# Kernel optimization log

Hardware: AMD Instinct MI355X
Metric: run time of the kernel (lower is better)

Reference implementation:

```python
import jax, jax.numpy as jnp
import numpy as np

D_MODEL = 1024
NUM_HEADS = 16
D_K = D_MODEL // NUM_HEADS
HEADS_DIST = [4, 4, 2, 2, 4]  # [token, statement, data_flow, control_flow, standard]
HYP_DF = 5.0
HYP_CF = 5.0
NEG_INF = -1000000000.0
B, S = 4, 1024


def _head_group_weights():
    # one-hot-per-group weight vectors of length NUM_HEADS
    ws = []
    start = 0
    for n in HEADS_DIST:
        w = np.zeros(NUM_HEADS, dtype=np.float32)
        w[start:start + n] = 1.0
        ws.append(jnp.asarray(w))
        start += n
    return ws  # tok_w, stmt_w, df_w, cf_w, std_w


def setup_inputs() -> dict:
    key = jax.random.key(0)
    ks = jax.random.split(key, 12)
    f32 = jnp.float32
    inp = {
        'Q': jax.random.normal(ks[0], (B, S, D_MODEL), f32),
        'K': jax.random.normal(ks[1], (B, S, D_MODEL), f32),
        'V': jax.random.normal(ks[2], (B, S, D_MODEL), f32),
        'token': jax.random.randint(ks[3], (B, S, S), 0, 2).astype(f32),
        'statement': jax.random.randint(ks[4], (B, S, S), 0, 2).astype(f32),
        'data_flow': jax.random.randint(ks[5], (B, S, S), 0, 2).astype(f32),
        'control_flow': jax.random.randint(ks[6], (B, S, S), 0, 2).astype(f32),
        'zero_matrix': jnp.zeros((B, S, S), f32),
        'mask': jax.random.randint(ks[7], (B, 1, S, S), 0, 2).astype(jnp.int32),
        # linear layer params (torch nn.Linear: y = x @ W.T + b)
        'Wq': jax.random.normal(ks[8], (D_MODEL, D_MODEL), f32) * 0.02,
        'bq': jnp.zeros((D_MODEL,), f32),
        'Wk': jax.random.normal(ks[9], (D_MODEL, D_MODEL), f32) * 0.02,
        'bk': jnp.zeros((D_MODEL,), f32),
        'Wv': jax.random.normal(ks[10], (D_MODEL, D_MODEL), f32) * 0.02,
        'bv': jnp.zeros((D_MODEL,), f32),
        'Wo': jax.random.normal(ks[11], (D_MODEL, D_MODEL), f32) * 0.02,
        'bo': jnp.zeros((D_MODEL,), f32),
    }
    return inp


def _split_heads(x):
    b, s, _ = x.shape
    return x.reshape(b, s, NUM_HEADS, D_K).transpose(0, 2, 1, 3)  # (B,H,S,dk)


def reference(Q, K, V, token, statement, data_flow, control_flow, zero_matrix,
              mask, Wq, bq, Wk, bk, Wv, bv, Wo, bo):
    tok_w, stmt_w, df_w, cf_w, _ = _head_group_weights()

    Qh = _split_heads(Q @ Wq.T + bq)
    Kh = _split_heads(K @ Wk.T + bk)
    Vh = _split_heads(V @ Wv.T + bv)

    scores = jnp.einsum('bhqd,bhkd->bhqk', Qh, Kh) / jnp.sqrt(jnp.float32(D_K))

    # local mask: -1e9 * token for token-heads, -1e9 * statement for statement-heads,
    # zero_matrix (zeros) elsewhere — expressed via per-head group weights instead of
    # the original redundant stack.
    w = lambda v: v[None, :, None, None]  # (1,H,1,1)
    local_mask = NEG_INF * (w(tok_w) * token[:, None] + w(stmt_w) * statement[:, None])
    # global enhance: |scores * (hyp_df*data_flow | hyp_cf*control_flow)| on their heads
    enhance_adj = (HYP_DF * w(df_w) * data_flow[:, None]
                   + HYP_CF * w(cf_w) * control_flow[:, None])
    global_enhance = jnp.abs(enhance_adj * scores)

    scores = scores + local_mask + global_enhance
    scores = jnp.where(mask == 0, NEG_INF, scores)

    probs = jax.nn.softmax(scores, axis=-1)  # (B,H,S,S)
    ctx = jnp.einsum('bhqk,bhkd->bhqd', probs, Vh)
    out = ctx.transpose(0, 2, 1, 3).reshape(B, S, D_MODEL)
    return out @ Wo.T + bo
```

## Files before the change

### kernel.cpp

```cpp
#include <hip/hip_runtime.h>
#include <stdint.h>

typedef unsigned short u16;
typedef unsigned int   u32;
typedef unsigned char  u8;
typedef __attribute__((ext_vector_type(4))) float f32x4;
typedef __attribute__((ext_vector_type(8))) __bf16 bf16x8;
typedef __attribute__((ext_vector_type(2))) unsigned int u32x2;
typedef __attribute__((ext_vector_type(4))) unsigned int u32x4;

#define MFMA16(a, b, c) __builtin_amdgcn_mfma_f32_16x16x32_bf16((a), (b), (c), 0, 0, 0)

__device__ __forceinline__ u16 f2bf(float f) {
  u32 u = __float_as_uint(f);
  return (u16)((u + 0x7fffu + ((u >> 16) & 1u)) >> 16);
}

__device__ __forceinline__ void gl_lds16(const void* g, void* l) {
  __builtin_amdgcn_global_load_lds((const __attribute__((address_space(1))) u32*)g,
                                   (__attribute__((address_space(3))) u32*)l, 16, 0, 0);
}

__device__ __forceinline__ u32 cvtpk(float a, float b) {
  u32 r;
  asm("v_cvt_pk_bf16_f32 %0, %1, %2" : "=v"(r) : "v"(a), "v"(b));
  return r;
}

__device__ __forceinline__ float exp2_hw(float x) {
  float r;
  asm("v_exp_f32 %0, %1" : "=v"(r) : "v"(x));
  return r;
}

__device__ __forceinline__ void plswap32(u32& x, u32& y) {
  u32x2 r = __builtin_amdgcn_permlane32_swap(x, y, false, false);
  x = r.x; y = r.y;
}
__device__ __forceinline__ void plswap16(u32& x, u32& y) {
  u32x2 r = __builtin_amdgcn_permlane16_swap(x, y, false, false);
  x = r.x; y = r.y;
}

__device__ __forceinline__ float redmax_lg(float v) {
  u32 x = __float_as_uint(v), y = x;
  plswap16(x, y);
  float m = fmaxf(__uint_as_float(x), __uint_as_float(y));
  u32 a = __float_as_uint(m), b = a;
  plswap32(a, b);
  return fmaxf(__uint_as_float(a), __uint_as_float(b));
}
__device__ __forceinline__ float redsum_lg(float v) {
  u32 x = __float_as_uint(v), y = x;
  plswap16(x, y);
  float m = __uint_as_float(x) + __uint_as_float(y);
  u32 a = __float_as_uint(m), b = a;
  plswap32(a, b);
  return __uint_as_float(a) + __uint_as_float(b);
}

__device__ __forceinline__ u32 pbit(float t, float s, float d, float c, int m) {
  const u32 nm = (m == 0) ? 1u : 0u;
  u32 r = (t != 0.0f ? 1u : 0u) | (s != 0.0f ? 2u : 0u) | (d != 0.0f ? 4u : 0u) |
          (c != 0.0f ? 8u : 0u) | ((1u - nm) << 4);
  r |= (((t != 0.0f ? 1u : 0u) | nm) << 5) | (((s != 0.0f ? 1u : 0u) | nm) << 6) | (nm << 7);
  return r;
}

__global__ void __launch_bounds__(256) prep_kernel(
    const float4* __restrict__ Q, const float4* __restrict__ K, const float4* __restrict__ V,
    const float4* __restrict__ Wq, const float4* __restrict__ Wk, const float4* __restrict__ Wv,
    const float4* __restrict__ Wo, ushort4* __restrict__ oQ, ushort4* __restrict__ oK,
    ushort4* __restrict__ oV, ushort4* __restrict__ oWq, ushort4* __restrict__ oWk,
    ushort4* __restrict__ oWv, ushort4* __restrict__ oWo,
    const float4* __restrict__ tok, const float4* __restrict__ st, const float4* __restrict__ df,
    const float4* __restrict__ cf, const int4* __restrict__ msk, u32* __restrict__ pko) {
  const int bid = blockIdx.x;
  float4 v;
  if (bid < 2048) {
    const int i = bid * 512 + threadIdx.x;
#pragma unroll
    for (int u = 0; u < 2; u++) {
      const int k = i + u * 256;
      v = Q[k]; oQ[k] = make_ushort4(f2bf(v.x), f2bf(v.y), f2bf(v.z), f2bf(v.w));
      v = K[k]; oK[k] = make_ushort4(f2bf(v.x), f2bf(v.y), f2bf(v.z), f2bf(v.w));
      v = V[k]; oV[k] = make_ushort4(f2bf(v.x), f2bf(v.y), f2bf(v.z), f2bf(v.w));
    }
  } else if (bid < 2560) {
    const int j = (bid - 2048) * 512 + threadIdx.x;
#pragma unroll
    for (int u = 0; u < 2; u++) {
      const int k = j + u * 256;
      v = Wq[k]; oWq[k] = make_ushort4(f2bf(v.x), f2bf(v.y), f2bf(v.z), f2bf(v.w));
      v = Wk[k]; oWk[k] = make_ushort4(f2bf(v.x), f2bf(v.y), f2bf(v.z), f2bf(v.w));
      v = Wv[k]; oWv[k] = make_ushort4(f2bf(v.x), f2bf(v.y), f2bf(v.z), f2bf(v.w));
      v = Wo[k]; oWo[k] = make_ushort4(f2bf(v.x), f2bf(v.y), f2bf(v.z), f2bf(v.w));
    }
  } else {
    const int i = (bid - 2560) * 256 + threadIdx.x;
    const int b = i >> 18, rem = i & 262143, q = rem >> 8, k4 = rem & 255;
    const int t = k4 >> 4, nk = (k4 >> 2) & 3, lg = k4 & 3;
    const u32 widx = ((u32)(b * 64 + (q >> 4)) * 16 + t) * 256 + (q & 15) * 16 + lg * 4 + nk;
    float4 vt = tok[i], vs = st[i], vd = df[i], vc = cf[i];
    int4 vm = msk[i];
    u32 b0 = pbit(vt.x, vs.x, vd.x, vc.x, vm.x);
    u32 b1 = pbit(vt.y, vs.y, vd.y, vc.y, vm.y);
    u32 b2 = pbit(vt.z, vs.z, vd.z, vc.z, vm.z);
    u32 b3 = pbit(vt.w, vs.w, vd.w, vc.w, vm.w);
    pko[widx] = b0 | (b1 << 8) | (b2 << 16) | (b3 << 24);
  }
}

__global__ void __launch_bounds__(256) gemm_qkv(const u16* __restrict__ Abase, const u16* __restrict__ Wbase,
                                                const float* __restrict__ bq, const float* __restrict__ bk,
                                                const float* __restrict__ bv, u16* __restrict__ Obase) {
  __shared__ u16 smA[128 * 32];
  __shared__ u16 smB[128 * 32];
  const int fb = blockIdx.x;
  const int lid = (fb & 7) * 96 + (fb >> 3);
  const int z = lid >> 8;
  const int m0 = ((lid & 255) >> 3) * 128;
  const int n0 = (lid & 7) * 128;
  const u16* A = Abase + (size_t)z * 4194304;
  const u16* W = Wbase + (size_t)z * 1048576;
  const float* bias = (z == 0) ? bq : (z == 1) ? bk : bv;
  u16* Out = Obase + (size_t)z * 4194304;
  const int t = threadIdx.x;
  const int w = t >> 6, l = t & 63;
  const int l15 = l & 15, lg = l >> 4;
  const int wr = w >> 1, wc = w & 1;
  f32x4 acc[4][4] = {};
  const int srow = w * 16 + (l >> 2);
  const int scol = (l & 3) * 8;
  const u16* Ab = A + (size_t)(m0 + srow) * 1024 + scol;
  const u16* Wb = W + (size_t)(n0 + srow) * 1024 + scol;
  u16* sA0 = smA + srow * 32 + scol;
  u16* sB0 = smB + srow * 32 + scol;
  for (int kk = 0; kk < 1024; kk += 32) {
    gl_lds16(Ab + kk, sA0);
    gl_lds16(Ab + kk + (size_t)64 * 1024, sA0 + 64 * 32);
    gl_lds16(Wb + kk, sB0);
    gl_lds16(Wb + kk + (size_t)64 * 1024, sB0 + 64 * 32);
    __syncthreads();
    bf16x8 af[4], bv_[4];
#pragma unroll
    for (int i = 0; i < 4; i++) af[i] = *(const bf16x8*)(smA + (wr * 64 + i * 16 + l15) * 32 + lg * 8);
#pragma unroll
    for (int i = 0; i < 4; i++) bv_[i] = *(const bf16x8*)(smB + (wc * 64 + i * 16 + l15) * 32 + lg * 8);
#pragma unroll
    for (int i = 0; i < 4; i++)
#pragma unroll
      for (int j = 0; j < 4; j++) acc[i][j] = MFMA16(af[i], bv_[j], acc[i][j]);
    __syncthreads();
  }
#pragma unroll
  for (int j = 0; j < 4; j++) {
    const int n = n0 + wc * 64 + j * 16 + l15;
    const float bvj = bias[n];
#pragma unroll
    for (int i = 0; i < 4; i++) {
      const int mbase = m0 + wr * 64 + i * 16 + lg * 4;
      if (z < 2) {
#pragma unroll
        for (int r = 0; r < 4; r++) {
          const int m = mbase + r;
          Out[((size_t)((m >> 10) * 16 + (n >> 6)) << 16) + (size_t)(m & 1023) * 64 + (n & 63)] =
              f2bf(acc[i][j][r] + bvj);
        }
      } else {
        size_t off = ((size_t)((mbase >> 10) * 16 + (n >> 6)) << 16) + (size_t)(n & 63) * 1024 + (mbase & 1023);
        *(ushort4*)(Out + off) = make_ushort4(f2bf(acc[i][j][0] + bvj), f2bf(acc[i][j][1] + bvj),
                                              f2bf(acc[i][j][2] + bvj), f2bf(acc[i][j][3] + bvj));
      }
    }
  }
}

__global__ void __launch_bounds__(256) gemm_out(const u16* __restrict__ A, const u16* __restrict__ W,
                                                const float* __restrict__ bias, float* __restrict__ Out) {
  __shared__ u16 smA[128 * 32];
  __shared__ u16 smB[128 * 32];
  const int fb = blockIdx.x;
  const int lid = (fb & 7) * 32 + (fb >> 3);
  const int m0 = (lid >> 3) * 128;
  const int n0 = (lid & 7) * 128;
  const int t = threadIdx.x;
  const int w = t >> 6, l = t & 63;
  const int l15 = l & 15, lg = l >> 4;
  const int wr = w >> 1, wc = w & 1;
  f32x4 acc[4][4] = {};
  const int srow = w * 16 + (l >> 2);
  const int scol = (l & 3) * 8;
  const u16* Ab = A + (size_t)(m0 + srow) * 1024 + scol;
  const u16* Wb = W + (size_t)(n0 + srow) * 1024 + scol;
  u16* sA0 = smA + srow * 32 + scol;
  u16* sB0 = smB + srow * 32 + scol;
  for (int kk = 0; kk < 1024; kk += 32) {
    gl_lds16(Ab + kk, sA0);
    gl_lds16(Ab + kk + (size_t)64 * 1024, sA0 + 64 * 32);
    gl_lds16(Wb + kk, sB0);
    gl_lds16(Wb + kk + (size_t)64 * 1024, sB0 + 64 * 32);
    __syncthreads();
    bf16x8 af[4], bv_[4];
#pragma unroll
    for (int i = 0; i < 4; i++) af[i] = *(const bf16x8*)(smA + (wr * 64 + i * 16 + l15) * 32 + lg * 8);
#pragma unroll
    for (int i = 0; i < 4; i++) bv_[i] = *(const bf16x8*)(smB + (wc * 64 + i * 16 + l15) * 32 + lg * 8);
#pragma unroll
    for (int i = 0; i < 4; i++)
#pragma unroll
      for (int j = 0; j < 4; j++) acc[i][j] = MFMA16(af[i], bv_[j], acc[i][j]);
    __syncthreads();
  }
#pragma unroll
  for (int j = 0; j < 4; j++) {
    const int n = n0 + wc * 64 + j * 16 + l15;
    const float bvj = bias[n];
#pragma unroll
    for (int i = 0; i < 4; i++) {
      const int mbase = m0 + wr * 64 + i * 16 + lg * 4;
#pragma unroll
      for (int r = 0; r < 4; r++) Out[(size_t)(mbase + r) * 1024 + n] = acc[i][j][r] + bvj;
    }
  }
}

__global__ void __launch_bounds__(256) attn_kernel(const u16* __restrict__ Qp, const u16* __restrict__ Kp,
                                                   const u16* __restrict__ Vt, const u8* __restrict__ pack,
                                                   u16* __restrict__ ctx) {
  __shared__ u16 smK[2][4096];
  __shared__ u16 smV[2][4096];
  const float SCL  = 0.18033688011112042f;
  const float NEGL = -1.44269504e9f;
  const int tid = threadIdx.x;
  const int w = tid >> 6, l = tid & 63;
  const int l15 = l & 15, lg = l >> 4;
  const int f = blockIdx.x;
  const int swz = (f & 7) * 128 + (f >> 3);
  const int bh = swz >> 4, bx = swz & 15;
  const int b = bh >> 4, h = bh & 15;
  const int q0 = bx * 64 + w * 16;
  const bool enh = (h >= 8 && h < 12);
  const u32 kbit = (h < 4) ? 0x20u : (h < 8) ? 0x40u : 0x80u;
  const u32 ebit = (h < 10) ? 0x04u : 0x08u;
  const u32 kb_[4] = {kbit, kbit << 8, kbit << 16, kbit << 24};
  const u32 eb_[4] = {ebit, ebit << 8, ebit << 16, ebit << 24};
  const size_t hb = (size_t)bh << 16;

  bf16x8 qf[2];
#pragma unroll
  for (int ks = 0; ks < 2; ks++)
    qf[ks] = *(const bf16x8*)(Qp + hb + (size_t)(q0 + l15) * 64 + ks * 32 + lg * 8);

  const int srow = w * 16 + (l >> 3);
  const int schunk = (l & 7) ^ (l >> 3);
  const u16* Ksrc = Kp + hb + (size_t)srow * 64 + schunk * 8;
  const u16* Vsrc = Vt + hb + (size_t)srow * 1024 + schunk * 8;
  const int c0 = (lg ^ (l15 & 7)) * 8;
  const u8* pkq = pack + ((size_t)((b * 64 + bx * 4 + w) * 16)) * 1024 + (l15 * 4 + lg) * 16;

  gl_lds16(Ksrc, &smK[0][w * 1024]);
  gl_lds16(Ksrc + 512, &smK[0][w * 1024 + 512]);
  gl_lds16(Vsrc, &smV[0][w * 1024]);
  gl_lds16(Vsrc + 8192, &smV[0][w * 1024 + 512]);
  uint4 pk_next = *(const uint4*)(pkq);

  f32x4 octx[4] = {};
  float mrun = -3.0e38f, lrun = 0.0f;

  for (int t = 0; t < 16; t++) {
    __syncthreads();
    const uint4 pkc = pk_next;
    if (t < 15) {
      const int kb = (t + 1) * 64;
      const int nb = (t + 1) & 1;
      gl_lds16(Ksrc + (size_t)kb * 64, &smK[nb][w * 1024]);
      gl_lds16(Ksrc + (size_t)kb * 64 + 512, &smK[nb][w * 1024 + 512]);
      gl_lds16(Vsrc + kb, &smV[nb][w * 1024]);
      gl_lds16(Vsrc + kb + 8192, &smV[nb][w * 1024 + 512]);
      pk_next = *(const uint4*)(pkq + (t + 1) * 1024);
    }
    const u16* bK = smK[t & 1];
    const u16* bV = smV[t & 1];
    f32x4 sc[4];
#pragma unroll
    for (int nk = 0; nk < 4; nk++) {
      const u16* kr = bK + (nk * 16 + l15) * 64;
      bf16x8 kf0 = *(const bf16x8*)(kr + c0);
      bf16x8 kf1 = *(const bf16x8*)(kr + (c0 ^ 32));
      f32x4 z = {0.0f, 0.0f, 0.0f, 0.0f};
      z = MFMA16(kf0, qf[0], z);
      z = MFMA16(kf1, qf[1], z);
      sc[nk] = z;
    }
    const u32 pkw[4] = {pkc.x, pkc.y, pkc.z, pkc.w};
#pragma unroll
    for (int nk = 0; nk < 4; nk++)
#pragma unroll
      for (int r = 0; r < 4; r++) {
        float s = sc[nk][r] * SCL;
        if (enh) s = (pkw[nk] & eb_[r]) ? __builtin_fmaf(fabsf(s), 5.0f, s) : s;
        sc[nk][r] = (pkw[nk] & kb_[r]) ? NEGL : s;
      }
    float mx[4];
#pragma unroll
    for (int nk = 0; nk < 4; nk++)
      mx[nk] = fmaxf(fmaxf(sc[nk][0], sc[nk][1]), fmaxf(sc[nk][2], sc[nk][3]));
    float smax = fmaxf(fmaxf(mx[0], mx[1]), fmaxf(mx[2], mx[3]));
    smax = redmax_lg(smax);
    const bool defer = __all(smax - mrun <= 11.0f);
    const float mn = defer ? mrun : fmaxf(mrun, smax);
    float psum = 0.0f;
#pragma unroll
    for (int nk = 0; nk < 4; nk++)
#pragma unroll
      for (int r = 0; r < 4; r++) {
        float p = exp2_hw(sc[nk][r] - mn);
        sc[nk][r] = p;
        psum += p;
      }
    psum = redsum_lg(psum);
    if (defer) {
      lrun += psum;
    } else {
      const float so = exp2_hw(mrun - mn);
      lrun = lrun * so + psum;
      mrun = mn;
#pragma unroll
      for (int nd = 0; nd < 4; nd++)
#pragma unroll
        for (int r = 0; r < 4; r++) octx[nd][r] *= so;
    }
#pragma unroll
    for (int kk = 0; kk < 2; kk++) {
      u32 a0 = cvtpk(sc[2 * kk][0], sc[2 * kk][1]);
      u32 a1 = cvtpk(sc[2 * kk][2], sc[2 * kk][3]);
      u32 b0 = cvtpk(sc[2 * kk + 1][0], sc[2 * kk + 1][1]);
      u32 b1 = cvtpk(sc[2 * kk + 1][2], sc[2 * kk + 1][3]);
      plswap32(a0, b0);
      plswap32(a1, b1);
      plswap16(a0, b0);
      plswap16(a1, b1);
      u32x4 wv = {a0, a1, b0, b1};
      bf16x8 pfrag = __builtin_bit_cast(bf16x8, wv);
#pragma unroll
      for (int nd = 0; nd < 4; nd++) {
        bf16x8 vf = *(const bf16x8*)(bV + (nd * 16 + l15) * 64 + (c0 ^ (kk * 32)));
        octx[nd] = MFMA16(vf, pfrag, octx[nd]);
      }
    }
  }
  const float inv = 1.0f / lrun;
  u16* cb = ctx + (size_t)b * 1048576 + (size_t)(q0 + l15) * 1024 + h * 64 + lg * 4;
#pragma unroll
  for (int nd = 0; nd < 4; nd++) {
    *(ushort4*)(cb + nd * 16) = make_ushort4(f2bf(octx[nd][0] * inv), f2bf(octx[nd][1] * inv),
                                             f2bf(octx[nd][2] * inv), f2bf(octx[nd][3] * inv));
  }
}

extern "C" void kernel_launch(void* const* d_in, const int* in_sizes, int n_in,
                              void* d_out, int out_size, void* d_ws, size_t ws_size,
                              hipStream_t stream) {
  (void)in_sizes; (void)n_in; (void)out_size; (void)ws_size;
  const float* Q  = (const float*)d_in[0];
  const float* K  = (const float*)d_in[1];
  const float* V  = (const float*)d_in[2];
  const float* tok = (const float*)d_in[3];
  const float* st  = (const float*)d_in[4];
  const float* df  = (const float*)d_in[5];
  const float* cf  = (const float*)d_in[6];
  const int*   msk = (const int*)d_in[8];
  const float* Wq = (const float*)d_in[9];
  const float* bq = (const float*)d_in[10];
  const float* Wk = (const float*)d_in[11];
  const float* bk = (const float*)d_in[12];
  const float* Wv = (const float*)d_in[13];
  const float* bv = (const float*)d_in[14];
  const float* Wo = (const float*)d_in[15];
  const float* bo = (const float*)d_in[16];

  char* ws = (char*)d_ws;
  const size_t MB = 1ull << 20;
  u16* Qbf = (u16*)(ws);
  u16* Wqb = (u16*)(ws + 24 * MB);
  u8*  pkQ = (u8*)(ws + 32 * MB);
  u16* Qh  = (u16*)(ws + 36 * MB);
  u16* ctx = (u16*)(ws + 60 * MB);
  u16* Kbf = Qbf + 4194304;
  u16* Vbf = Qbf + 8388608;
  u16* Wkb = Wqb + 1048576;
  u16* Wvb = Wqb + 2097152;
  u16* Wob = Wqb + 3145728;

  prep_kernel<<<6656, 256, 0, stream>>>(
      (const float4*)Q, (const float4*)K, (const float4*)V, (const float4*)Wq, (const float4*)Wk,
      (const float4*)Wv, (const float4*)Wo, (ushort4*)Qbf, (ushort4*)Kbf, (ushort4*)Vbf,
      (ushort4*)Wqb, (ushort4*)Wkb, (ushort4*)Wvb, (ushort4*)Wob,
      (const float4*)tok, (const float4*)st, (const float4*)df, (const float4*)cf,
      (const int4*)msk, (u32*)pkQ);
  gemm_qkv<<<768, 256, 0, stream>>>(Qbf, Wqb, bq, bk, bv, Qh);
  attn_kernel<<<1024, 256, 0, stream>>>(Qh, Qh + 4194304, Qh + 8388608, pkQ, ctx);
  gemm_out<<<256, 256, 0, stream>>>(ctx, Wob, bo, (float*)d_out);
}
```

Before: 148.8 us.

## Fuse fp32-to-bf16 conversion into GEMM loads with register prefetch

Removes the separate prep pass that converted Q/K/V and all weights to bf16. The QKV and output GEMMs now read fp32 directly into registers, convert to bf16, and store to LDS. The next tile is prefetched into registers during the MFMA work, and the loop barrier is restructured. This saves a full extra read and write of the activations and weights, but the GEMMs now read twice as many bytes from global memory and replace direct global-to-LDS loads with register staging.

```diff
diff --git a/kernel.cpp b/kernel.cpp
--- a/kernel.cpp
+++ b/kernel.cpp
@@ -67,51 +67,25 @@
   return r;
 }
 
-__global__ void __launch_bounds__(256) prep_kernel(
-    const float4* __restrict__ Q, const float4* __restrict__ K, const float4* __restrict__ V,
-    const float4* __restrict__ Wq, const float4* __restrict__ Wk, const float4* __restrict__ Wv,
-    const float4* __restrict__ Wo, ushort4* __restrict__ oQ, ushort4* __restrict__ oK,
-    ushort4* __restrict__ oV, ushort4* __restrict__ oWq, ushort4* __restrict__ oWk,
-    ushort4* __restrict__ oWv, ushort4* __restrict__ oWo,
-    const float4* __restrict__ tok, const float4* __restrict__ st, const float4* __restrict__ df,
-    const float4* __restrict__ cf, const int4* __restrict__ msk, u32* __restrict__ pko) {
-  const int bid = blockIdx.x;
-  float4 v;
-  if (bid < 2048) {
-    const int i = bid * 512 + threadIdx.x;
-#pragma unroll
-    for (int u = 0; u < 2; u++) {
-      const int k = i + u * 256;
-      v = Q[k]; oQ[k] = make_ushort4(f2bf(v.x), f2bf(v.y), f2bf(v.z), f2bf(v.w));
-      v = K[k]; oK[k] = make_ushort4(f2bf(v.x), f2bf(v.y), f2bf(v.z), f2bf(v.w));
-      v = V[k]; oV[k] = make_ushort4(f2bf(v.x), f2bf(v.y), f2bf(v.z), f2bf(v.w));
-    }
-  } else if (bid < 2560) {
-    const int j = (bid - 2048) * 512 + threadIdx.x;
-#pragma unroll
-    for (int u = 0; u < 2; u++) {
-      const int k = j + u * 256;
-      v = Wq[k]; oWq[k] = make_ushort4(f2bf(v.x), f2bf(v.y), f2bf(v.z), f2bf(v.w));
-      v = Wk[k]; oWk[k] = make_ushort4(f2bf(v.x), f2bf(v.y), f2bf(v.z), f2bf(v.w));
-      v = Wv[k]; oWv[k] = make_ushort4(f2bf(v.x), f2bf(v.y), f2bf(v.z), f2bf(v.w));
-      v = Wo[k]; oWo[k] = make_ushort4(f2bf(v.x), f2bf(v.y), f2bf(v.z), f2bf(v.w));
-    }
-  } else {
-    const int i = (bid - 2560) * 256 + threadIdx.x;
-    const int b = i >> 18, rem = i & 262143, q = rem >> 8, k4 = rem & 255;
-    const int t = k4 >> 4, nk = (k4 >> 2) & 3, lg = k4 & 3;
-    const u32 widx = ((u32)(b * 64 + (q >> 4)) * 16 + t) * 256 + (q & 15) * 16 + lg * 4 + nk;
-    float4 vt = tok[i], vs = st[i], vd = df[i], vc = cf[i];
-    int4 vm = msk[i];
-    u32 b0 = pbit(vt.x, vs.x, vd.x, vc.x, vm.x);
-    u32 b1 = pbit(vt.y, vs.y, vd.y, vc.y, vm.y);
-    u32 b2 = pbit(vt.z, vs.z, vd.z, vc.z, vm.z);
-    u32 b3 = pbit(vt.w, vs.w, vd.w, vc.w, vm.w);
-    pko[widx] = b0 | (b1 << 8) | (b2 << 16) | (b3 << 24);
-  }
-}
-
-__global__ void __launch_bounds__(256) gemm_qkv(const u16* __restrict__ Abase, const u16* __restrict__ Wbase,
+__global__ void __launch_bounds__(256) pack_kernel(const float4* __restrict__ tok, const float4* __restrict__ st,
+                                                   const float4* __restrict__ df, const float4* __restrict__ cf,
+                                                   const int4* __restrict__ msk, u32* __restrict__ pko) {
+  const int i = blockIdx.x * 256 + threadIdx.x;
+  const int b = i >> 18, rem = i & 262143, q = rem >> 8, k4 = rem & 255;
+  const int t = k4 >> 4, nk = (k4 >> 2) & 3, lg = k4 & 3;
+  const u32 widx = ((u32)(b * 64 + (q >> 4)) * 16 + t) * 256 + (q & 15) * 16 + lg * 4 + nk;
+  float4 vt = tok[i], vs = st[i], vd = df[i], vc = cf[i];
+  int4 vm = msk[i];
+  u32 b0 = pbit(vt.x, vs.x, vd.x, vc.x, vm.x);
+  u32 b1 = pbit(vt.y, vs.y, vd.y, vc.y, vm.y);
+  u32 b2 = pbit(vt.z, vs.z, vd.z, vc.z, vm.z);
+  u32 b3 = pbit(vt.w, vs.w, vd.w, vc.w, vm.w);
+  pko[widx] = b0 | (b1 << 8) | (b2 << 16) | (b3 << 24);
+}
+
+__global__ void __launch_bounds__(256) gemm_qkv(const float* __restrict__ Qf, const float* __restrict__ Kf,
+                                                const float* __restrict__ Vf, const float* __restrict__ Wqf,
+                                                const float* __restrict__ Wkf, const float* __restrict__ Wvf,
                                                 const float* __restrict__ bq, const float* __restrict__ bk,
                                                 const float* __restrict__ bv, u16* __restrict__ Obase) {
   __shared__ u16 smA[128 * 32];
@@ -121,8 +95,8 @@
   const int z = lid >> 8;
   const int m0 = ((lid & 255) >> 3) * 128;
   const int n0 = (lid & 7) * 128;
-  const u16* A = Abase + (size_t)z * 4194304;
-  const u16* W = Wbase + (size_t)z * 1048576;
+  const float* A = (z == 0) ? Qf : (z == 1) ? Kf : Vf;
+  const float* W = (z == 0) ? Wqf : (z == 1) ? Wkf : Wvf;
   const float* bias = (z == 0) ? bq : (z == 1) ? bk : bv;
   u16* Out = Obase + (size_t)z * 4194304;
   const int t = threadIdx.x;
@@ -132,16 +106,41 @@
   f32x4 acc[4][4] = {};
   const int srow = w * 16 + (l >> 2);
   const int scol = (l & 3) * 8;
-  const u16* Ab = A + (size_t)(m0 + srow) * 1024 + scol;
-  const u16* Wb = W + (size_t)(n0 + srow) * 1024 + scol;
+  const float* Ab = A + (size_t)(m0 + srow) * 1024 + scol;
+  const float* Wb = W + (size_t)(n0 + srow) * 1024 + scol;
   u16* sA0 = smA + srow * 32 + scol;
   u16* sB0 = smB + srow * 32 + scol;
+
+  float4 ra[2][2], rb[2][2];
+#pragma unroll
+  for (int p = 0; p < 2; p++)
+#pragma unroll
+    for (int hf = 0; hf < 2; hf++) {
+      ra[p][hf] = *(const float4*)(Ab + p * 65536 + hf * 4);
+      rb[p][hf] = *(const float4*)(Wb + p * 65536 + hf * 4);
+    }
+
   for (int kk = 0; kk < 1024; kk += 32) {
-    gl_lds16(Ab + kk, sA0);
-    gl_lds16(Ab + kk + (size_t)64 * 1024, sA0 + 64 * 32);
-    gl_lds16(Wb + kk, sB0);
-    gl_lds16(Wb + kk + (size_t)64 * 1024, sB0 + 64 * 32);
     __syncthreads();
+#pragma unroll
+    for (int p = 0; p < 2; p++) {
+      u32x4 wa = {cvtpk(ra[p][0].x, ra[p][0].y), cvtpk(ra[p][0].z, ra[p][0].w),
+                  cvtpk(ra[p][1].x, ra[p][1].y), cvtpk(ra[p][1].z, ra[p][1].w)};
+      *(u32x4*)(sA0 + p * 2048) = wa;
+      u32x4 wb2 = {cvtpk(rb[p][0].x, rb[p][0].y), cvtpk(rb[p][0].z, rb[p][0].w),
+                   cvtpk(rb[p][1].x, rb[p][1].y), cvtpk(rb[p][1].z, rb[p][1].w)};
+      *(u32x4*)(sB0 + p * 2048) = wb2;
+    }
+    __syncthreads();
+    if (kk < 992) {
+#pragma unroll
+      for (int p = 0; p < 2; p++)
+#pragma unroll
+        for (int hf = 0; hf < 2; hf++) {
+          ra[p][hf] = *(const float4*)(Ab + kk + 32 + p * 65536 + hf * 4);
+          rb[p][hf] = *(const float4*)(Wb + kk + 32 + p * 65536 + hf * 4);
+        }
+    }
     bf16x8 af[4], bv_[4];
 #pragma unroll
     for (int i = 0; i < 4; i++) af[i] = *(const bf16x8*)(smA + (wr * 64 + i * 16 + l15) * 32 + lg * 8);
@@ -151,7 +150,6 @@
     for (int i = 0; i < 4; i++)
 #pragma unroll
       for (int j = 0; j < 4; j++) acc[i][j] = MFMA16(af[i], bv_[j], acc[i][j]);
-    __syncthreads();
   }
 #pragma unroll
   for (int j = 0; j < 4; j++) {
@@ -176,7 +174,7 @@
   }
 }
 
-__global__ void __launch_bounds__(256) gemm_out(const u16* __restrict__ A, const u16* __restrict__ W,
+__global__ void __launch_bounds__(256) gemm_out(const u16* __restrict__ A, const float* __restrict__ W,
                                                 const float* __restrict__ bias, float* __restrict__ Out) {
   __shared__ u16 smA[128 * 32];
   __shared__ u16 smB[128 * 32];
@@ -192,15 +190,33 @@
   const int srow = w * 16 + (l >> 2);
   const int scol = (l & 3) * 8;
   const u16* Ab = A + (size_t)(m0 + srow) * 1024 + scol;
-  const u16* Wb = W + (size_t)(n0 + srow) * 1024 + scol;
+  const float* Wb = W + (size_t)(n0 + srow) * 1024 + scol;
   u16* sA0 = smA + srow * 32 + scol;
   u16* sB0 = smB + srow * 32 + scol;
+
+  float4 rb[2][2];
+#pragma unroll
+  for (int p = 0; p < 2; p++)
+#pragma unroll
+    for (int hf = 0; hf < 2; hf++) rb[p][hf] = *(const float4*)(Wb + p * 65536 + hf * 4);
+
   for (int kk = 0; kk < 1024; kk += 32) {
+    __syncthreads();
     gl_lds16(Ab + kk, sA0);
     gl_lds16(Ab + kk + (size_t)64 * 1024, sA0 + 64 * 32);
-    gl_lds16(Wb + kk, sB0);
-    gl_lds16(Wb + kk + (size_t)64 * 1024, sB0 + 64 * 32);
+#pragma unroll
+    for (int p = 0; p < 2; p++) {
+      u32x4 wb2 = {cvtpk(rb[p][0].x, rb[p][0].y), cvtpk(rb[p][0].z, rb[p][0].w),
+                   cvtpk(rb[p][1].x, rb[p][1].y), cvtpk(rb[p][1].z, rb[p][1].w)};
+      *(u32x4*)(sB0 + p * 2048) = wb2;
+    }
     __syncthreads();
+    if (kk < 992) {
+#pragma unroll
+      for (int p = 0; p < 2; p++)
+#pragma unroll
+        for (int hf = 0; hf < 2; hf++) rb[p][hf] = *(const float4*)(Wb + kk + 32 + p * 65536 + hf * 4);
+    }
     bf16x8 af[4], bv_[4];
 #pragma unroll
     for (int i = 0; i < 4; i++) af[i] = *(const bf16x8*)(smA + (wr * 64 + i * 16 + l15) * 32 + lg * 8);
@@ -210,7 +226,6 @@
     for (int i = 0; i < 4; i++)
 #pragma unroll
       for (int j = 0; j < 4; j++) acc[i][j] = MFMA16(af[i], bv_[j], acc[i][j]);
-    __syncthreads();
   }
 #pragma unroll
   for (int j = 0; j < 4; j++) {
@@ -382,24 +397,13 @@
 
   char* ws = (char*)d_ws;
   const size_t MB = 1ull << 20;
-  u16* Qbf = (u16*)(ws);
-  u16* Wqb = (u16*)(ws + 24 * MB);
-  u8*  pkQ = (u8*)(ws + 32 * MB);
-  u16* Qh  = (u16*)(ws + 36 * MB);
-  u16* ctx = (u16*)(ws + 60 * MB);
-  u16* Kbf = Qbf + 4194304;
-  u16* Vbf = Qbf + 8388608;
-  u16* Wkb = Wqb + 1048576;
-  u16* Wvb = Wqb + 2097152;
-  u16* Wob = Wqb + 3145728;
-
-  prep_kernel<<<6656, 256, 0, stream>>>(
-      (const float4*)Q, (const float4*)K, (const float4*)V, (const float4*)Wq, (const float4*)Wk,
-      (const float4*)Wv, (const float4*)Wo, (ushort4*)Qbf, (ushort4*)Kbf, (ushort4*)Vbf,
-      (ushort4*)Wqb, (ushort4*)Wkb, (ushort4*)Wvb, (ushort4*)Wob,
-      (const float4*)tok, (const float4*)st, (const float4*)df, (const float4*)cf,
-      (const int4*)msk, (u32*)pkQ);
-  gemm_qkv<<<768, 256, 0, stream>>>(Qbf, Wqb, bq, bk, bv, Qh);
+  u8*  pkQ = (u8*)(ws);
+  u16* Qh  = (u16*)(ws + 4 * MB);
+  u16* ctx = (u16*)(ws + 28 * MB);
+
+  pack_kernel<<<4096, 256, 0, stream>>>((const float4*)tok, (const float4*)st, (const float4*)df,
+                                        (const float4*)cf, (const int4*)msk, (u32*)pkQ);
+  gemm_qkv<<<768, 256, 0, stream>>>(Q, K, V, Wq, Wk, Wv, bq, bk, bv, Qh);
   attn_kernel<<<1024, 256, 0, stream>>>(Qh, Qh + 4194304, Qh + 8388608, pkQ, ctx);
-  gemm_out<<<256, 256, 0, stream>>>(ctx, Wob, bo, (float*)d_out);
-}
+  gemm_out<<<256, 256, 0, stream>>>(ctx, Wo, bo, (float*)d_out);
+}
```

New measurement: 139.4 us. 1.07x faster.
